# Kernel tuning notes

Measured on AMD Instinct MI355X. Metric: run time of the kernel, lower is better.

## Reference

```python
import jax, jax.numpy as jnp
import numpy as np

NH = 8  # num_heads
CHUNK = 32  # query-block size for chunked L1 cdist


def _mlp(x, w1, b1, w2, b2, w3, b3):
    h = jax.nn.relu(x @ w1 + b1)
    h = jax.nn.relu(h @ w2 + b2)
    return h @ w3 + b3


def _split_heads(x, nh):
    # Faithful to source: reshape last dim as (d, nh) then permute -> [B, nh, S, d]
    B, S, H = x.shape
    return jnp.transpose(x.reshape(B, S, H // nh, nh), (0, 3, 1, 2))


def _cdist_l1(K, Q, chunk=CHUNK):
    # torch.cdist(K, Q, p=1): D[b,h,i,j] = sum_d |K[b,h,i,d] - Q[b,h,j,d]|
    # Chunk over query rows to bound the broadcasted |K-Q| intermediate.
    B, h, Sq, d = Q.shape
    Sk = K.shape[2]
    Qb = jnp.moveaxis(Q.reshape(B, h, Sq // chunk, chunk, d), 2, 0)  # [nb,B,h,chunk,d]

    def block(q):  # q: [B,h,chunk,d]
        return jnp.sum(jnp.abs(K[:, :, :, None, :] - q[:, :, None, :, :]), axis=-1)  # [B,h,Sk,chunk]

    D = jax.lax.map(block, Qb)  # [nb,B,h,Sk,chunk]
    return jnp.moveaxis(D, 0, 3).reshape(B, h, Sk, Sq)


def setup_inputs() -> dict:
    key = jax.random.key(0)
    ks = jax.random.split(key, 32)
    B, S, F, H, O = 4, 1024, 128, 512, 128
    s = 0.02

    def lin(i, fin, fout):
        return (jax.random.normal(ks[i], (fin, fout), jnp.float32) * s,
                jnp.zeros((fout,), jnp.float32))

    inp = {
        'KEY': jax.random.normal(ks[0], (B, S, F), jnp.float32),
        'VALUE': jax.random.normal(ks[1], (B, S, F), jnp.float32),
        'QUERY': jax.random.normal(ks[2], (B, S, F), jnp.float32),
    }
    idx = 3
    for n in ['k', 'q', 'v']:
        for li, (fin, fout) in enumerate([(F, H), (H, H), (H, H)], 1):
            w, b = lin(idx, fin, fout); idx += 1
            inp[f'W{n}_w{li}'] = w
            inp[f'W{n}_b{li}'] = b
    w, b = lin(idx, H, O)
    inp['Wo_w'] = w
    inp['Wo_b'] = b
    return inp


def reference(KEY, VALUE, QUERY,
              Wk_w1, Wk_b1, Wk_w2, Wk_b2, Wk_w3, Wk_b3,
              Wq_w1, Wq_b1, Wq_w2, Wq_b2, Wq_w3, Wq_b3,
              Wv_w1, Wv_b1, Wv_w2, Wv_b2, Wv_w3, Wv_b3,
              Wo_w, Wo_b):
    Wk = _split_heads(_mlp(KEY, Wk_w1, Wk_b1, Wk_w2, Wk_b2, Wk_w3, Wk_b3), NH)   # [B,h,Sk,d]
    Wq = _split_heads(_mlp(QUERY, Wq_w1, Wq_b1, Wq_w2, Wq_b2, Wq_w3, Wq_b3), NH)  # [B,h,Sq,d]
    Wv = _split_heads(_mlp(VALUE, Wv_w1, Wv_b1, Wv_w2, Wv_b2, Wv_w3, Wv_b3), NH)  # [B,h,Sk,d]

    D = _cdist_l1(Wk, Wq)                              # [B,h,Sk,Sq]
    attn = jax.nn.softmax(-(D * D) * 0.5, axis=1)      # softmax over HEAD axis, as in source
    out = jnp.einsum('bhik,bhij->bhjk', attn, Wv)      # [B,h,d,Sq]
    B, h, d, Sq = out.shape
    out = jnp.transpose(out, (0, 2, 1, 3)).reshape(B, d * h, Sq)  # [B,hidden,Sq]
    out = jnp.transpose(out, (0, 2, 1))                # [B,Sq,hidden]
    return out @ Wo_w + Wo_b                           # dropout = identity (eval)
```

## Files before the change

### kernel.cpp

```cpp
#include <hip/hip_runtime.h>
#include <hip/hip_bf16.h>
#include <hip/hip_fp16.h>

typedef unsigned short u16;
typedef __attribute__((ext_vector_type(8))) short short8;
typedef __attribute__((ext_vector_type(4))) float floatx4;

#define DEVI static __device__ __forceinline__

DEVI float bf2f(u16 b) { return __uint_as_float(((unsigned)b) << 16); }
DEVI u16 f2bf(float f) {
  __hip_bfloat16 h = __float2bfloat16(f);
  u16 u; __builtin_memcpy(&u, &h, 2); return u;
}
DEVI u16 f2h(float f) {
  __half h = __float2half(f);
  u16 u; __builtin_memcpy(&u, &h, 2); return u;
}

template <int CTRL>
DEVI float dpp_add_f(float v) {
  int i; __builtin_memcpy(&i, &v, 4);
  int p = __builtin_amdgcn_update_dpp(0, i, CTRL, 0xF, 0xF, false);
  float pv; __builtin_memcpy(&pv, &p, 4);
  return v + pv;
}

DEVI int hperm(int f) { return ((f & 7) << 6) | (f >> 3); }

struct TransArgs {
  const float* src[10];
  u16* dst[10];
  int R[10];
  int C[10];
};

__global__ __launch_bounds__(256) void transpose_k(TransArgs t) {
  const int z = blockIdx.z;
  const float* __restrict__ src = t.src[z];
  u16* __restrict__ dst = t.dst[z];
  const int R = t.R[z], C = t.C[z];
  const int c0 = blockIdx.x * 32, r0 = blockIdx.y * 32;
  if (c0 >= C || r0 >= R) return;
  __shared__ float tile[32][33];
  const int tx = threadIdx.x & 31, ty = threadIdx.x >> 5;
  for (int i = ty; i < 32; i += 8)
    tile[i][tx] = src[(size_t)(r0 + i) * C + c0 + tx];
  __syncthreads();
  for (int i = ty; i < 32; i += 8) {
    const int f = r0 + tx;
    const int fi = (z == 9) ? hperm(f) : f;
    dst[(size_t)(c0 + i) * R + fi] = f2bf(tile[tx][i]);
  }
}

struct GemmArgs {
  const void* A[3];
  const u16* WT[3];
  const float* bias[3];
  void* C[3];
};

__global__ __launch_bounds__(256) void gemm_bias_act(GemmArgs ga, int M, int N, int K,
                                                     int relu, int a_f32, int c_mode,
                                                     int out_perm) {
  const int z = blockIdx.z;
  const void* __restrict__ A = ga.A[z];
  const u16* __restrict__ WT = ga.WT[z];
  const float* __restrict__ bias = ga.bias[z];
  void* __restrict__ C = ga.C[z];

  __shared__ u16 As[64][72];
  __shared__ u16 Bs[64][72];

  const int tid = threadIdx.x;
  const int lane = tid & 63;
  const int wave = tid >> 6;
  const int wm = wave >> 1, wn = wave & 1;
  const int mb = blockIdx.y, nb = blockIdx.x;

  floatx4 acc0 = {0.f, 0.f, 0.f, 0.f}, acc1 = acc0, acc2 = acc0, acc3 = acc0;

  const int sr = tid >> 3;
  const int sc = (tid & 7) * 8;

  for (int k0 = 0; k0 < K; k0 += 64) {
    __syncthreads();
#pragma unroll
    for (int it = 0; it < 2; ++it) {
      const int rr = sr + it * 32;
      if (a_f32) {
        const float* Af = (const float*)A;
        const float4 f0 = *(const float4*)(Af + (size_t)(mb * 64 + rr) * K + k0 + sc);
        const float4 f1 = *(const float4*)(Af + (size_t)(mb * 64 + rr) * K + k0 + sc + 4);
        u16 tmp[8] = {f2bf(f0.x), f2bf(f0.y), f2bf(f0.z), f2bf(f0.w),
                      f2bf(f1.x), f2bf(f1.y), f2bf(f1.z), f2bf(f1.w)};
        int4 t; __builtin_memcpy(&t, tmp, 16);
        *(int4*)&As[rr][sc] = t;
      } else {
        const u16* Ab = (const u16*)A;
        *(int4*)&As[rr][sc] = *(const int4*)(Ab + (size_t)(mb * 64 + rr) * K + k0 + sc);
      }
      *(int4*)&Bs[rr][sc] = *(const int4*)(WT + (size_t)(nb * 64 + rr) * K + k0 + sc);
    }
    __syncthreads();
#pragma unroll
    for (int ks = 0; ks < 2; ++ks) {
      const int koff = ks * 32 + (lane >> 4) * 8;
      const int am = wm * 32 + (lane & 15);
      const int bn = wn * 32 + (lane & 15);
      short8 a0 = *(const short8*)&As[am][koff];
      short8 a1 = *(const short8*)&As[am + 16][koff];
      short8 b0 = *(const short8*)&Bs[bn][koff];
      short8 b1 = *(const short8*)&Bs[bn + 16][koff];
      acc0 = __builtin_amdgcn_mfma_f32_16x16x32_bf16(a0, b0, acc0, 0, 0, 0);
      acc1 = __builtin_amdgcn_mfma_f32_16x16x32_bf16(a0, b1, acc1, 0, 0, 0);
      acc2 = __builtin_amdgcn_mfma_f32_16x16x32_bf16(a1, b0, acc2, 0, 0, 0);
      acc3 = __builtin_amdgcn_mfma_f32_16x16x32_bf16(a1, b1, acc3, 0, 0, 0);
    }
  }

  const int colb = nb * 64 + wn * 32 + (lane & 15);
  const int rowb = mb * 64 + wm * 32 + (lane >> 4) * 4;
  const floatx4 accs[4] = {acc0, acc1, acc2, acc3};
#pragma unroll
  for (int mg = 0; mg < 2; ++mg) {
#pragma unroll
    for (int ng = 0; ng < 2; ++ng) {
      const int col = colb + ng * 16;
      const float bv = bias[col];
      const int colw = out_perm ? hperm(col) : col;
      const floatx4 v = accs[mg * 2 + ng];
#pragma unroll
      for (int r = 0; r < 4; ++r) {
        const int row = rowb + mg * 16 + r;
        float x = v[r] + bv;
        if (relu) x = fmaxf(x, 0.f);
        if (c_mode == 1)      ((float*)C)[(size_t)row * N + colw] = x;
        else if (c_mode == 2) ((u16*)C)[(size_t)row * N + colw] = f2h(x);
        else                  ((u16*)C)[(size_t)row * N + colw] = f2bf(x);
      }
    }
  }
}

__global__ __launch_bounds__(256, 2) void attn_kernel(const u16* __restrict__ Km,
                                                      const u16* __restrict__ Qm,
                                                      const u16* __restrict__ Vm,
                                                      u16* __restrict__ partial) {
  __shared__ alignas(16) u16 lds[4 * 2048];

  const int tid = threadIdx.x;
  const int lane = tid & 63;
  const int wave = tid >> 6;
  const int wid = blockIdx.x * 4 + wave;
  const int qt = wid & 63;
  const int sp = (wid >> 6) & 7;
  const int b = wid >> 9;
  const int j0 = qt * 16;

  const int qg = lane >> 4;
  const int h = (lane >> 1) & 7;
  const int half = lane & 1;

  int grans[4];
#pragma unroll
  for (int pi = 0; pi < 4; ++pi)
    grans[pi] = h * 8 + half * 4 + ((pi + h) & 3);

  int4 Qr[4][4];
#pragma unroll
  for (int qi = 0; qi < 4; ++qi) {
    const u16* qrow = Qm + (size_t)(b * 1024 + j0 + qg + qi * 4) * 512;
#pragma unroll
    for (int pi = 0; pi < 4; ++pi)
      Qr[qi][pi] = *(const int4*)(qrow + grans[pi] * 8);
  }

  __half2 o[4][4][4];
#pragma unroll
  for (int qi = 0; qi < 4; ++qi)
#pragma unroll
    for (int pi = 0; pi < 4; ++pi)
#pragma unroll
      for (int j = 0; j < 4; ++j) o[qi][pi][j] = __float2half2_rn(0.f);

  u16* Kw = lds + wave * 2048;
  u16* Vw = Kw + 1024;
  const int keyBase = b * 1024 + sp * 128;

  int4 Kp[2], Vp[2];
#pragma unroll
  for (int r = 0; r < 2; ++r) {
    const size_t ga = (size_t)(keyBase + r) * 512 + lane * 8;
    Kp[r] = *(const int4*)(Km + ga);
    Vp[r] = *(const int4*)(Vm + ga);
  }

#pragma unroll 1
  for (int t = 0; t < 64; ++t) {
#pragma unroll
    for (int r = 0; r < 2; ++r) {
      *(int4*)(Kw + r * 512 + lane * 8) = Kp[r];
      *(int4*)(Vw + r * 512 + lane * 8) = Vp[r];
    }
    if (t < 63) {
#pragma unroll
      for (int r = 0; r < 2; ++r) {
        const size_t ga = (size_t)(keyBase + (t + 1) * 2 + r) * 512 + lane * 8;
        Kp[r] = *(const int4*)(Km + ga);
        Vp[r] = *(const int4*)(Vm + ga);
      }
    }

#pragma unroll
    for (int r = 0; r < 2; ++r) {
      const u16* krow = Kw + r * 512;
      __half2 acc[4][2];
#pragma unroll
      for (int qi = 0; qi < 4; ++qi) {
        acc[qi][0] = __float2half2_rn(0.f);
        acc[qi][1] = __float2half2_rn(0.f);
      }
#pragma unroll
      for (int pi = 0; pi < 4; ++pi) {
        const int4 kv = *(const int4*)(krow + grans[pi] * 8);
        const __half2* kh = reinterpret_cast<const __half2*>(&kv);
#pragma unroll
        for (int qi = 0; qi < 4; ++qi) {
          const __half2* qh = reinterpret_cast<const __half2*>(&Qr[qi][pi]);
          acc[qi][0] = __hadd2(acc[qi][0], __habs2(__hsub2(kh[0], qh[0])));
          acc[qi][1] = __hadd2(acc[qi][1], __habs2(__hsub2(kh[1], qh[1])));
          acc[qi][0] = __hadd2(acc[qi][0], __habs2(__hsub2(kh[2], qh[2])));
          acc[qi][1] = __hadd2(acc[qi][1], __habs2(__hsub2(kh[3], qh[3])));
        }
      }

      __half2 wh[4];
#pragma unroll
      for (int qi = 0; qi < 4; ++qi) {
        const __half2 s2 = __hadd2(acc[qi][0], acc[qi][1]);
        float d8p = __half2float(__low2half(s2)) + __half2float(__high2half(s2));
        const float d8 = dpp_add_f<0xB1>(d8p);
        const float e = __expf(-0.5f * d8 * d8);
        float nrm = e;
        nrm = dpp_add_f<0x4E>(nrm);
        nrm = dpp_add_f<0x141>(nrm);
        nrm = dpp_add_f<0x140>(nrm);
        const float w = e * __builtin_amdgcn_rcpf(nrm);
        wh[qi] = __float2half2_rn(w);
      }

      const u16* vrow = Vw + r * 512;
#pragma unroll
      for (int pi = 0; pi < 4; ++pi) {
        const int4 vv = *(const int4*)(vrow + grans[pi] * 8);
        const __half2* vh = reinterpret_cast<const __half2*>(&vv);
#pragma unroll
        for (int qi = 0; qi < 4; ++qi) {
          o[qi][pi][0] = __hfma2(wh[qi], vh[0], o[qi][pi][0]);
          o[qi][pi][1] = __hfma2(wh[qi], vh[1], o[qi][pi][1]);
          o[qi][pi][2] = __hfma2(wh[qi], vh[2], o[qi][pi][2]);
          o[qi][pi][3] = __hfma2(wh[qi], vh[3], o[qi][pi][3]);
        }
      }
    }
  }

#pragma unroll
  for (int qi = 0; qi < 4; ++qi) {
    const int j = j0 + qg + qi * 4;
    u16* dst = partial + (size_t)sp * (4096 * 512) + (size_t)(b * 1024 + j) * 512;
#pragma unroll
    for (int pi = 0; pi < 4; ++pi) {
      int4 pk; __builtin_memcpy(&pk, &o[qi][pi][0], 16);
      *(int4*)(dst + grans[pi] * 8) = pk;
    }
  }
}

__global__ __launch_bounds__(256) void reduce_k(const u16* __restrict__ p,
                                                u16* __restrict__ out) {
  const size_t i = ((size_t)blockIdx.x * 256 + threadIdx.x) * 8;
  float s[8] = {0.f, 0.f, 0.f, 0.f, 0.f, 0.f, 0.f, 0.f};
#pragma unroll
  for (int sp = 0; sp < 8; ++sp) {
    const int4 t = *(const int4*)(p + (size_t)sp * (4096 * 512) + i);
    const __half* th = reinterpret_cast<const __half*>(&t);
#pragma unroll
    for (int j = 0; j < 8; ++j) s[j] += __half2float(th[j]);
  }
  int4 pk;
  u16* pu = reinterpret_cast<u16*>(&pk);
#pragma unroll
  for (int j = 0; j < 8; ++j) pu[j] = f2bf(s[j]);
  *(int4*)(out + i) = pk;
}

extern "C" void kernel_launch(void* const* d_in, const int* in_sizes, int n_in,
                              void* d_out, int out_size, void* d_ws, size_t ws_size,
                              hipStream_t stream) {
  (void)in_sizes; (void)n_in; (void)out_size; (void)ws_size;
  char* wsp = (char*)d_ws;
  size_t off = 0;
  auto take = [&](size_t bytes) {
    void* p = (void*)(wsp + off);
    off += ((bytes + 255) & ~(size_t)255);
    return p;
  };

  static const int wR[10] = {128, 512, 512, 128, 512, 512, 128, 512, 512, 512};
  static const int wC[10] = {512, 512, 512, 512, 512, 512, 512, 512, 512, 128};
  static const int widx[10] = {3, 5, 7, 9, 11, 13, 15, 17, 19, 21};

  u16* WT[10];
  for (int i = 0; i < 10; ++i) WT[i] = (u16*)take((size_t)wR[i] * wC[i] * 2);
  u16* h1[3]; for (int i = 0; i < 3; ++i) h1[i] = (u16*)take((size_t)4096 * 512 * 2);
  u16* h2[3]; for (int i = 0; i < 3; ++i) h2[i] = (u16*)take((size_t)4096 * 512 * 2);
  u16* partial = (u16*)take((size_t)8 * 4096 * 512 * 2);

  TransArgs ta;
  for (int i = 0; i < 10; ++i) {
    ta.src[i] = (const float*)d_in[widx[i]];
    ta.dst[i] = WT[i];
    ta.R[i] = wR[i];
    ta.C[i] = wC[i];
  }
  hipLaunchKernelGGL(transpose_k, dim3(16, 16, 10), dim3(256), 0, stream, ta);

  GemmArgs g1 = {};
  g1.A[0] = d_in[0]; g1.A[1] = d_in[2]; g1.A[2] = d_in[1];
  g1.WT[0] = WT[0]; g1.WT[1] = WT[3]; g1.WT[2] = WT[6];
  g1.bias[0] = (const float*)d_in[4]; g1.bias[1] = (const float*)d_in[10]; g1.bias[2] = (const float*)d_in[16];
  g1.C[0] = h1[0]; g1.C[1] = h1[1]; g1.C[2] = h1[2];
  hipLaunchKernelGGL(gemm_bias_act, dim3(8, 64, 3), dim3(256), 0, stream, g1, 4096, 512, 128, 1, 1, 0, 0);

  GemmArgs g2 = {};
  for (int i = 0; i < 3; ++i) { g2.A[i] = h1[i]; g2.C[i] = h2[i]; }
  g2.WT[0] = WT[1]; g2.WT[1] = WT[4]; g2.WT[2] = WT[7];
  g2.bias[0] = (const float*)d_in[6]; g2.bias[1] = (const float*)d_in[12]; g2.bias[2] = (const float*)d_in[18];
  hipLaunchKernelGGL(gemm_bias_act, dim3(8, 64, 3), dim3(256), 0, stream, g2, 4096, 512, 512, 1, 0, 0, 0);

  GemmArgs g3 = {};
  for (int i = 0; i < 3; ++i) { g3.A[i] = h2[i]; g3.C[i] = h1[i]; }
  g3.WT[0] = WT[2]; g3.WT[1] = WT[5]; g3.WT[2] = WT[8];
  g3.bias[0] = (const float*)d_in[8]; g3.bias[1] = (const float*)d_in[14]; g3.bias[2] = (const float*)d_in[20];
  hipLaunchKernelGGL(gemm_bias_act, dim3(8, 64, 3), dim3(256), 0, stream, g3, 4096, 512, 512, 0, 0, 2, 1);

  hipLaunchKernelGGL(attn_kernel, dim3(512), dim3(256), 0, stream, h1[0], h1[1], h1[2], partial);

  hipLaunchKernelGGL(reduce_k, dim3(1024), dim3(256), 0, stream, partial, h2[0]);

  GemmArgs g4 = {};
  g4.A[0] = h2[0]; g4.WT[0] = WT[9]; g4.bias[0] = (const float*)d_in[22]; g4.C[0] = d_out;
  hipLaunchKernelGGL(gemm_bias_act, dim3(2, 64, 1), dim3(256), 0, stream, g4, 4096, 128, 512, 0, 0, 1, 0);
}
```

Measured before the change: 401.0 us.

## Enlarge GEMM tiles to 128x128, pre-convert inputs, split attention keys 16 ways

Replaces the 64x64 GEMM with a 128x128-tile variant using 16 MFMA accumulators per wave, moving fp32-to-bf16 input conversion into a separate kernel. Attention now splits keys into 16 chunks of 64 instead of 8 chunks of 128, doubling grid size and raising launch bounds to 4 blocks per CU. This aims for more MFMA reuse per LDS load and more parallelism in attention, at the cost of fewer GEMM blocks, an extra conversion pass, and twice the partial-sum traffic in the reduce step.

```diff
diff --git a/kernel.cpp b/kernel.cpp
--- a/kernel.cpp
+++ b/kernel.cpp
@@ -54,24 +54,41 @@
   }
 }
 
+struct ConvArgs {
+  const float* src[3];
+  u16* dst[3];
+};
+
+__global__ __launch_bounds__(256) void conv_k(ConvArgs c) {
+  const int z = blockIdx.z;
+  const float* __restrict__ src = c.src[z];
+  u16* __restrict__ dst = c.dst[z];
+  const size_t i = ((size_t)blockIdx.x * 256 + threadIdx.x) * 8;
+  const float4 f0 = *(const float4*)(src + i);
+  const float4 f1 = *(const float4*)(src + i + 4);
+  u16 tmp[8] = {f2bf(f0.x), f2bf(f0.y), f2bf(f0.z), f2bf(f0.w),
+                f2bf(f1.x), f2bf(f1.y), f2bf(f1.z), f2bf(f1.w)};
+  int4 t; __builtin_memcpy(&t, tmp, 16);
+  *(int4*)(dst + i) = t;
+}
+
 struct GemmArgs {
-  const void* A[3];
+  const u16* A[3];
   const u16* WT[3];
   const float* bias[3];
   void* C[3];
 };
 
-__global__ __launch_bounds__(256) void gemm_bias_act(GemmArgs ga, int M, int N, int K,
-                                                     int relu, int a_f32, int c_mode,
-                                                     int out_perm) {
+__global__ __launch_bounds__(256, 2) void gemm128(GemmArgs ga, int M, int N, int K,
+                                                  int relu, int c_mode, int out_perm) {
   const int z = blockIdx.z;
-  const void* __restrict__ A = ga.A[z];
+  const u16* __restrict__ A = ga.A[z];
   const u16* __restrict__ WT = ga.WT[z];
   const float* __restrict__ bias = ga.bias[z];
   void* __restrict__ C = ga.C[z];
 
-  __shared__ u16 As[64][72];
-  __shared__ u16 Bs[64][72];
+  __shared__ u16 As[128][72];
+  __shared__ u16 Bs[128][72];
 
   const int tid = threadIdx.x;
   const int lane = tid & 63;
@@ -79,7 +96,11 @@
   const int wm = wave >> 1, wn = wave & 1;
   const int mb = blockIdx.y, nb = blockIdx.x;
 
-  floatx4 acc0 = {0.f, 0.f, 0.f, 0.f}, acc1 = acc0, acc2 = acc0, acc3 = acc0;
+  floatx4 acc[4][4];
+#pragma unroll
+  for (int mi = 0; mi < 4; ++mi)
+#pragma unroll
+    for (int ni = 0; ni < 4; ++ni) acc[mi][ni] = floatx4{0.f, 0.f, 0.f, 0.f};
 
   const int sr = tid >> 3;
   const int sc = (tid & 7) * 8;
@@ -87,53 +108,40 @@
   for (int k0 = 0; k0 < K; k0 += 64) {
     __syncthreads();
 #pragma unroll
-    for (int it = 0; it < 2; ++it) {
+    for (int it = 0; it < 4; ++it) {
       const int rr = sr + it * 32;
-      if (a_f32) {
-        const float* Af = (const float*)A;
-        const float4 f0 = *(const float4*)(Af + (size_t)(mb * 64 + rr) * K + k0 + sc);
-        const float4 f1 = *(const float4*)(Af + (size_t)(mb * 64 + rr) * K + k0 + sc + 4);
-        u16 tmp[8] = {f2bf(f0.x), f2bf(f0.y), f2bf(f0.z), f2bf(f0.w),
-                      f2bf(f1.x), f2bf(f1.y), f2bf(f1.z), f2bf(f1.w)};
-        int4 t; __builtin_memcpy(&t, tmp, 16);
-        *(int4*)&As[rr][sc] = t;
-      } else {
-        const u16* Ab = (const u16*)A;
-        *(int4*)&As[rr][sc] = *(const int4*)(Ab + (size_t)(mb * 64 + rr) * K + k0 + sc);
-      }
-      *(int4*)&Bs[rr][sc] = *(const int4*)(WT + (size_t)(nb * 64 + rr) * K + k0 + sc);
+      *(int4*)&As[rr][sc] = *(const int4*)(A + (size_t)(mb * 128 + rr) * K + k0 + sc);
+      *(int4*)&Bs[rr][sc] = *(const int4*)(WT + (size_t)(nb * 128 + rr) * K + k0 + sc);
     }
     __syncthreads();
 #pragma unroll
     for (int ks = 0; ks < 2; ++ks) {
       const int koff = ks * 32 + (lane >> 4) * 8;
-      const int am = wm * 32 + (lane & 15);
-      const int bn = wn * 32 + (lane & 15);
-      short8 a0 = *(const short8*)&As[am][koff];
-      short8 a1 = *(const short8*)&As[am + 16][koff];
-      short8 b0 = *(const short8*)&Bs[bn][koff];
-      short8 b1 = *(const short8*)&Bs[bn + 16][koff];
-      acc0 = __builtin_amdgcn_mfma_f32_16x16x32_bf16(a0, b0, acc0, 0, 0, 0);
-      acc1 = __builtin_amdgcn_mfma_f32_16x16x32_bf16(a0, b1, acc1, 0, 0, 0);
-      acc2 = __builtin_amdgcn_mfma_f32_16x16x32_bf16(a1, b0, acc2, 0, 0, 0);
-      acc3 = __builtin_amdgcn_mfma_f32_16x16x32_bf16(a1, b1, acc3, 0, 0, 0);
-    }
-  }
-
-  const int colb = nb * 64 + wn * 32 + (lane & 15);
-  const int rowb = mb * 64 + wm * 32 + (lane >> 4) * 4;
-  const floatx4 accs[4] = {acc0, acc1, acc2, acc3};
-#pragma unroll
-  for (int mg = 0; mg < 2; ++mg) {
-#pragma unroll
-    for (int ng = 0; ng < 2; ++ng) {
-      const int col = colb + ng * 16;
+      short8 af[4], bf[4];
+#pragma unroll
+      for (int i = 0; i < 4; ++i) {
+        af[i] = *(const short8*)&As[wm * 64 + i * 16 + (lane & 15)][koff];
+        bf[i] = *(const short8*)&Bs[wn * 64 + i * 16 + (lane & 15)][koff];
+      }
+#pragma unroll
+      for (int mi = 0; mi < 4; ++mi)
+#pragma unroll
+        for (int ni = 0; ni < 4; ++ni)
+          acc[mi][ni] = __builtin_amdgcn_mfma_f32_16x16x32_bf16(af[mi], bf[ni], acc[mi][ni], 0, 0, 0);
+    }
+  }
+
+#pragma unroll
+  for (int mi = 0; mi < 4; ++mi)
+#pragma unroll
+    for (int ni = 0; ni < 4; ++ni) {
+      const int col = nb * 128 + wn * 64 + ni * 16 + (lane & 15);
       const float bv = bias[col];
       const int colw = out_perm ? hperm(col) : col;
-      const floatx4 v = accs[mg * 2 + ng];
+      const floatx4 v = acc[mi][ni];
 #pragma unroll
       for (int r = 0; r < 4; ++r) {
-        const int row = rowb + mg * 16 + r;
+        const int row = mb * 128 + wm * 64 + mi * 16 + (lane >> 4) * 4 + r;
         float x = v[r] + bv;
         if (relu) x = fmaxf(x, 0.f);
         if (c_mode == 1)      ((float*)C)[(size_t)row * N + colw] = x;
@@ -141,10 +149,9 @@
         else                  ((u16*)C)[(size_t)row * N + colw] = f2bf(x);
       }
     }
-  }
-}
-
-__global__ __launch_bounds__(256, 2) void attn_kernel(const u16* __restrict__ Km,
+}
+
+__global__ __launch_bounds__(256, 4) void attn_kernel(const u16* __restrict__ Km,
                                                       const u16* __restrict__ Qm,
                                                       const u16* __restrict__ Vm,
                                                       u16* __restrict__ partial) {
@@ -155,8 +162,8 @@
   const int wave = tid >> 6;
   const int wid = blockIdx.x * 4 + wave;
   const int qt = wid & 63;
-  const int sp = (wid >> 6) & 7;
-  const int b = wid >> 9;
+  const int sp = (wid >> 6) & 15;
+  const int b = wid >> 10;
   const int j0 = qt * 16;
 
   const int qg = lane >> 4;
@@ -187,7 +194,7 @@
 
   u16* Kw = lds + wave * 2048;
   u16* Vw = Kw + 1024;
-  const int keyBase = b * 1024 + sp * 128;
+  const int keyBase = b * 1024 + sp * 64;
 
   int4 Kp[2], Vp[2];
 #pragma unroll
@@ -198,13 +205,13 @@
   }
 
 #pragma unroll 1
-  for (int t = 0; t < 64; ++t) {
+  for (int t = 0; t < 32; ++t) {
 #pragma unroll
     for (int r = 0; r < 2; ++r) {
       *(int4*)(Kw + r * 512 + lane * 8) = Kp[r];
       *(int4*)(Vw + r * 512 + lane * 8) = Vp[r];
     }
-    if (t < 63) {
+    if (t < 31) {
 #pragma unroll
       for (int r = 0; r < 2; ++r) {
         const size_t ga = (size_t)(keyBase + (t + 1) * 2 + r) * 512 + lane * 8;
@@ -284,7 +291,7 @@
   const size_t i = ((size_t)blockIdx.x * 256 + threadIdx.x) * 8;
   float s[8] = {0.f, 0.f, 0.f, 0.f, 0.f, 0.f, 0.f, 0.f};
 #pragma unroll
-  for (int sp = 0; sp < 8; ++sp) {
+  for (int sp = 0; sp < 16; ++sp) {
     const int4 t = *(const int4*)(p + (size_t)sp * (4096 * 512) + i);
     const __half* th = reinterpret_cast<const __half*>(&t);
 #pragma unroll
@@ -315,9 +322,10 @@
 
   u16* WT[10];
   for (int i = 0; i < 10; ++i) WT[i] = (u16*)take((size_t)wR[i] * wC[i] * 2);
+  u16* a0[3]; for (int i = 0; i < 3; ++i) a0[i] = (u16*)take((size_t)4096 * 128 * 2);
   u16* h1[3]; for (int i = 0; i < 3; ++i) h1[i] = (u16*)take((size_t)4096 * 512 * 2);
   u16* h2[3]; for (int i = 0; i < 3; ++i) h2[i] = (u16*)take((size_t)4096 * 512 * 2);
-  u16* partial = (u16*)take((size_t)8 * 4096 * 512 * 2);
+  u16* partial = (u16*)take((size_t)16 * 4096 * 512 * 2);
 
   TransArgs ta;
   for (int i = 0; i < 10; ++i) {
@@ -328,30 +336,35 @@
   }
   hipLaunchKernelGGL(transpose_k, dim3(16, 16, 10), dim3(256), 0, stream, ta);
 
+  ConvArgs ca;
+  ca.src[0] = (const float*)d_in[0]; ca.src[1] = (const float*)d_in[2]; ca.src[2] = (const float*)d_in[1];
+  ca.dst[0] = a0[0]; ca.dst[1] = a0[1]; ca.dst[2] = a0[2];
+  hipLaunchKernelGGL(conv_k, dim3(256, 1, 3), dim3(256), 0, stream, ca);
+
   GemmArgs g1 = {};
-  g1.A[0] = d_in[0]; g1.A[1] = d_in[2]; g1.A[2] = d_in[1];
+  for (int i = 0; i < 3; ++i) g1.A[i] = a0[i];
   g1.WT[0] = WT[0]; g1.WT[1] = WT[3]; g1.WT[2] = WT[6];
   g1.bias[0] = (const float*)d_in[4]; g1.bias[1] = (const float*)d_in[10]; g1.bias[2] = (const float*)d_in[16];
   g1.C[0] = h1[0]; g1.C[1] = h1[1]; g1.C[2] = h1[2];
-  hipLaunchKernelGGL(gemm_bias_act, dim3(8, 64, 3), dim3(256), 0, stream, g1, 4096, 512, 128, 1, 1, 0, 0);
+  hipLaunchKernelGGL(gemm128, dim3(4, 32, 3), dim3(256), 0, stream, g1, 4096, 512, 128, 1, 0, 0);
 
   GemmArgs g2 = {};
   for (int i = 0; i < 3; ++i) { g2.A[i] = h1[i]; g2.C[i] = h2[i]; }
   g2.WT[0] = WT[1]; g2.WT[1] = WT[4]; g2.WT[2] = WT[7];
   g2.bias[0] = (const float*)d_in[6]; g2.bias[1] = (const float*)d_in[12]; g2.bias[2] = (const float*)d_in[18];
-  hipLaunchKernelGGL(gemm_bias_act, dim3(8, 64, 3), dim3(256), 0, stream, g2, 4096, 512, 512, 1, 0, 0, 0);
+  hipLaunchKernelGGL(gemm128, dim3(4, 32, 3), dim3(256), 0, stream, g2, 4096, 512, 512, 1, 0, 0);
 
   GemmArgs g3 = {};
-  for (int i = 0; i < 3; ++i) { g3.A[i] = h2[i]; g3.C[i] = h1[i]; }
+  for (int i = 0; i < 3; ++i) { g3.A[i] = h2[i]; g3.C[i] = (void*)h1[i]; }
   g3.WT[0] = WT[2]; g3.WT[1] = WT[5]; g3.WT[2] = WT[8];
   g3.bias[0] = (const float*)d_in[8]; g3.bias[1] = (const float*)d_in[14]; g3.bias[2] = (const float*)d_in[20];
-  hipLaunchKernelGGL(gemm_bias_act, dim3(8, 64, 3), dim3(256), 0, stream, g3, 4096, 512, 512, 0, 0, 2, 1);
-
-  hipLaunchKernelGGL(attn_kernel, dim3(512), dim3(256), 0, stream, h1[0], h1[1], h1[2], partial);
+  hipLaunchKernelGGL(gemm128, dim3(4, 32, 3), dim3(256), 0, stream, g3, 4096, 512, 512, 0, 2, 1);
+
+  hipLaunchKernelGGL(attn_kernel, dim3(1024), dim3(256), 0, stream, h1[0], h1[1], h1[2], partial);
 
   hipLaunchKernelGGL(reduce_k, dim3(1024), dim3(256), 0, stream, partial, h2[0]);
 
   GemmArgs g4 = {};
   g4.A[0] = h2[0]; g4.WT[0] = WT[9]; g4.bias[0] = (const float*)d_in[22]; g4.C[0] = d_out;
-  hipLaunchKernelGGL(gemm_bias_act, dim3(2, 64, 1), dim3(256), 0, stream, g4, 4096, 128, 512, 0, 0, 1, 0);
-}
+  hipLaunchKernelGGL(gemm128, dim3(1, 32, 1), dim3(256), 0, stream, g4, 4096, 128, 512, 0, 1, 0);
+}
```

New measurement: 676.8 us. +68.8%, slower.
